# Kernel optimization log

Hardware: AMD Instinct MI355X
Metric: run time of the kernel (lower is better)

The kernel has to match this reference:

```python
import jax, jax.numpy as jnp
import numpy as np

FEAT = 1024
SUPPORT = 512
N = 4096


def setup_inputs() -> dict:
    key = jax.random.key(0)
    k1, k2, k3, k4, k5, k6 = jax.random.split(key, 6)
    s = 1.0 / np.sqrt(FEAT)
    f = jax.random.normal(k1, (N, FEAT), dtype=jnp.float32)
    G = jax.random.normal(k2, (SUPPORT, FEAT), dtype=jnp.float32)
    # PyTorch LSTMCell params: weight_ih [4*hidden, input], weight_hh [4*hidden, hidden]
    W_ih = jax.random.uniform(k3, (4 * FEAT, 2 * FEAT), minval=-s, maxval=s, dtype=jnp.float32)
    W_hh = jax.random.uniform(k4, (4 * FEAT, FEAT), minval=-s, maxval=s, dtype=jnp.float32)
    b_ih = jax.random.uniform(k5, (4 * FEAT,), minval=-s, maxval=s, dtype=jnp.float32)
    b_hh = jax.random.uniform(k6, (4 * FEAT,), minval=-s, maxval=s, dtype=jnp.float32)
    return {"f": f, "G": G, "W_ih": W_ih, "W_hh": W_hh, "b_ih": b_ih, "b_hh": b_hh, "n_ways": 20}


def _lstm_cell(x, h, c, W_ih, W_hh, b_ih, b_hh):
    # gates ordered i, f, g, o as in torch.nn.LSTMCell
    gates = x @ W_ih.T + b_ih + h @ W_hh.T + b_hh  # [N, 4*FEAT]
    i, fg, g, o = jnp.split(gates, 4, axis=1)
    i = jax.nn.sigmoid(i)
    fg = jax.nn.sigmoid(fg)
    g = jnp.tanh(g)
    o = jax.nn.sigmoid(o)
    c_new = fg * c + i * g
    h_new = o * jnp.tanh(c_new)
    return h_new, c_new


def reference(f, G, W_ih, W_hh, b_ih, b_hh, n_ways):
    h = f
    c = jnp.zeros_like(f)  # c_0 expanded, zeros (non-learned Variable)
    for _ in range(n_ways):
        logit_a = h @ G.T                      # [N, M]
        a = jax.nn.softmax(logit_a, axis=0)    # softmax over dim 0, as in original
        r = a @ G                              # [N, FEAT]
        x = jnp.concatenate((f, r), axis=1)    # [N, 2*FEAT]
        h, c = _lstm_cell(x, h, c, W_ih, W_hh, b_ih, b_hh)
        h = h + f
    return h
```

## Files before the change

kernel.cpp:

```cpp
#include <hip/hip_runtime.h>
#include <math.h>

#define NB    4096
#define FEAT  1024
#define MSUP  512
#define G4    4096
#define NWAYS 20

typedef _Float16 f16;
typedef f16 f16x8 __attribute__((ext_vector_type(8)));
typedef f16 f16x4 __attribute__((ext_vector_type(4)));
typedef float f32x4 __attribute__((ext_vector_type(4)));
typedef unsigned int u32;
#define GLOBAL_AS __attribute__((address_space(1)))
#define LDS_AS    __attribute__((address_space(3)))

__device__ __forceinline__ void load_lds16(const void* g, void* l) {
    __builtin_amdgcn_global_load_lds((const GLOBAL_AS u32*)g, (LDS_AS u32*)l, 16, 0, 0);
}

__device__ __forceinline__ float sigm(float x) { return 1.f / (1.f + __expf(-x)); }

template<int BM, int BN, int WROWS, int WCOLS, bool OUTF16, bool HASBIAS>
__global__ __launch_bounds__(256) void mfma_nt(
    void* __restrict__ Cv, int ldc,
    const f16* __restrict__ A1, int lda1, const f16* __restrict__ B1, int ldb1, int K1,
    const f16* __restrict__ A2, int lda2, const f16* __restrict__ B2, int ldb2, int K2,
    const f16* __restrict__ A3, int lda3, const f16* __restrict__ B3, int ldb3, int K3,
    const float* __restrict__ bias)
{
    constexpr int BK = 32;
    constexpr int WM = BM / WROWS, WN = BN / WCOLS;
    constexpr int FM = WM / 16,   FN = WN / 16;
    __shared__ f16 As[BM][BK];
    __shared__ f16 Bs[BN][BK];
    const int tid  = threadIdx.x;
    const int lane = tid & 63;
    const int wrow = (tid >> 6) % WROWS, wcol = (tid >> 6) / WROWS;
    const int bm = blockIdx.y * BM, bn = blockIdx.x * BN;
    const int lr = lane & 15, lq = lane >> 4;

    f32x4 acc[FM][FN] = {};

    #pragma unroll
    for (int pass = 0; pass < 3; ++pass) {
        const f16* A = pass == 0 ? A1 : (pass == 1 ? A2 : A3);
        const f16* B = pass == 0 ? B1 : (pass == 1 ? B2 : B3);
        const int lda = pass == 0 ? lda1 : (pass == 1 ? lda2 : lda3);
        const int ldb = pass == 0 ? ldb1 : (pass == 1 ? ldb2 : ldb3);
        const int K   = pass == 0 ? K1  : (pass == 1 ? K2  : K3);
        if (!A) break;
        #pragma unroll 1
        for (int k0 = 0; k0 < K; k0 += BK) {
            __syncthreads();
            #pragma unroll
            for (int t = 0; t < (BM * 4) / 256; ++t) {
                int c = t * 256 + tid;
                load_lds16(A + (size_t)(bm + (c >> 2)) * lda + k0 + (c & 3) * 8,
                           &As[0][0] + ((size_t)t * 256 + (tid & 192)) * 8);
            }
            #pragma unroll
            for (int t = 0; t < (BN * 4) / 256; ++t) {
                int c = t * 256 + tid;
                load_lds16(B + (size_t)(bn + (c >> 2)) * ldb + k0 + (c & 3) * 8,
                           &Bs[0][0] + ((size_t)t * 256 + (tid & 192)) * 8);
            }
            __syncthreads();
            f16x8 af[FM], bf[FN];
            #pragma unroll
            for (int i = 0; i < FM; ++i)
                af[i] = *(const f16x8*)&As[wrow * WM + i * 16 + lr][lq * 8];
            #pragma unroll
            for (int j = 0; j < FN; ++j)
                bf[j] = *(const f16x8*)&Bs[wcol * WN + j * 16 + lr][lq * 8];
            #pragma unroll
            for (int i = 0; i < FM; ++i)
                #pragma unroll
                for (int j = 0; j < FN; ++j)
                    acc[i][j] = __builtin_amdgcn_mfma_f32_16x16x32_f16(af[i], bf[j], acc[i][j], 0, 0, 0);
        }
    }

    #pragma unroll
    for (int i = 0; i < FM; ++i) {
        #pragma unroll
        for (int j = 0; j < FN; ++j) {
            const int col  = bn + wcol * WN + j * 16 + lr;
            const int row0 = bm + wrow * WM + i * 16 + lq * 4;
            float badd = HASBIAS ? bias[col] : 0.f;
            #pragma unroll
            for (int r = 0; r < 4; ++r) {
                size_t off = (size_t)(row0 + r) * ldc + col;
                float v = acc[i][j][r] + badd;
                if (OUTF16) ((f16*)Cv)[off] = (f16)v;
                else        ((float*)Cv)[off] = v;
            }
        }
    }
}

__global__ __launch_bounds__(512, 2) void gates_8p(
    const f16* __restrict__ a,
    const f16* __restrict__ h,
    const f16* __restrict__ Wcat,
    const f16* __restrict__ pre,
    const float* __restrict__ fin,
    float* __restrict__ cbuf,
    f16* __restrict__ hh,
    float* __restrict__ hout,
    int first, int writeH)
{
    extern __shared__ f16x8 smem8[];
    f16* smem = (f16*)smem8;
    const int tid  = threadIdx.x;
    const int lane = tid & 63;
    const int wid  = tid >> 6;
    const int wrow = wid >> 2, wcol = wid & 3;
    const int lr = lane & 15, lq = lane >> 4;

    const int bidr = blockIdx.y * 16 + blockIdx.x;
    const int wg   = (bidr & 7) * 32 + (bidr >> 3);
    const int bm = (wg >> 4) * 256;
    const int bn = (wg & 15) * 256;

    f32x4 acc[8][4] = {};

    auto stage = [&](const f16* src, int ld, int rb, int ko, f16* lbase, int l) {
        int c = l * 512 + tid;
        int r = c >> 3;
        int x = (c & 7) ^ (r & 7);
        load_lds16(src + (size_t)(rb + r) * ld + ko + (x << 3),
                   lbase + ((size_t)(l * 512 + (tid & 448))) * 8);
    };
    #define RDF(BUF, RB, KK) \
        (*(const f16x8*)((BUF) + ((size_t)((RB) + lr) << 6) + ((((KK) << 2 | lq) ^ (lr & 7)) << 3)))

    #pragma unroll
    for (int l = 0; l < 4; ++l) {
        stage(a,    MSUP, bm, 0, smem,         l);
        stage(Wcat, 2048, bn, 0, smem + 16384, l);
    }

    #pragma unroll 1
    for (int t = 0; t < 32; ++t) {
        f16* Ab = smem + (t & 1) * 32768;
        f16* Bb = Ab + 16384;
        f16* An = smem + ((t + 1) & 1) * 32768;
        f16* Bn = An + 16384;
        const int k1 = (t + 1) * 64;
        const f16* As2 = a; int lda2 = MSUP, ko2 = k1;
        if (k1 >= 1024)     { As2 = h; lda2 = FEAT; ko2 = k1 - 1024; }
        else if (k1 >= 512) { ko2 = k1 - 512; }
        const bool st = (t < 31);

        f16x8 af[4][2], bf[2][2], bg[2][2];

        if (st) {
            stage(As2, lda2, bm, ko2, An, 0);
            stage(Wcat, 2048, bn, k1, Bn, 0);
            asm volatile("s_waitcnt vmcnt(2)" ::: "memory");
        } else {
            asm volatile("s_waitcnt vmcnt(0)" ::: "memory");
        }
        asm volatile("s_barrier" ::: "memory");
        #pragma unroll
        for (int i = 0; i < 4; ++i)
            #pragma unroll
            for (int kk = 0; kk < 2; ++kk)
                af[i][kk] = RDF(Ab, wrow * 128 + i * 16, kk);
        #pragma unroll
        for (int j = 0; j < 2; ++j)
            #pragma unroll
            for (int kk = 0; kk < 2; ++kk)
                bf[j][kk] = RDF(Bb, wcol * 64 + j * 16, kk);
        __builtin_amdgcn_s_setprio(1);
        #pragma unroll
        for (int kk = 0; kk < 2; ++kk)
            #pragma unroll
            for (int i = 0; i < 4; ++i)
                #pragma unroll
                for (int j = 0; j < 2; ++j)
                    acc[i][j] = __builtin_amdgcn_mfma_f32_16x16x32_f16(af[i][kk], bf[j][kk], acc[i][j], 0, 0, 0);
        __builtin_amdgcn_s_setprio(0);
        __builtin_amdgcn_s_barrier();

        if (st) { stage(As2, lda2, bm, ko2, An, 1); stage(Wcat, 2048, bn, k1, Bn, 1); }
        #pragma unroll
        for (int j = 0; j < 2; ++j)
            #pragma unroll
            for (int kk = 0; kk < 2; ++kk)
                bg[j][kk] = RDF(Bb, wcol * 64 + (j + 2) * 16, kk);
        __builtin_amdgcn_s_barrier();
        __builtin_amdgcn_s_setprio(1);
        #pragma unroll
        for (int kk = 0; kk < 2; ++kk)
            #pragma unroll
            for (int i = 0; i < 4; ++i)
                #pragma unroll
                for (int j = 0; j < 2; ++j)
                    acc[i][j + 2] = __builtin_amdgcn_mfma_f32_16x16x32_f16(af[i][kk], bg[j][kk], acc[i][j + 2], 0, 0, 0);
        __builtin_amdgcn_s_setprio(0);
        __builtin_amdgcn_s_barrier();

        if (st) { stage(As2, lda2, bm, ko2, An, 2); stage(Wcat, 2048, bn, k1, Bn, 2); }
        #pragma unroll
        for (int i = 0; i < 4; ++i)
            #pragma unroll
            for (int kk = 0; kk < 2; ++kk)
                af[i][kk] = RDF(Ab, wrow * 128 + (i + 4) * 16, kk);
        __builtin_amdgcn_s_barrier();
        __builtin_amdgcn_s_setprio(1);
        #pragma unroll
        for (int kk = 0; kk < 2; ++kk)
            #pragma unroll
            for (int i = 0; i < 4; ++i)
                #pragma unroll
                for (int j = 0; j < 2; ++j)
                    acc[i + 4][j + 2] = __builtin_amdgcn_mfma_f32_16x16x32_f16(af[i][kk], bg[j][kk], acc[i + 4][j + 2], 0, 0, 0);
        __builtin_amdgcn_s_setprio(0);
        __builtin_amdgcn_s_barrier();

        if (st) { stage(As2, lda2, bm, ko2, An, 3); stage(Wcat, 2048, bn, k1, Bn, 3); }
        #pragma unroll
        for (int j = 0; j < 2; ++j)
            #pragma unroll
            for (int kk = 0; kk < 2; ++kk)
                bf[j][kk] = RDF(Bb, wcol * 64 + j * 16, kk);
        __builtin_amdgcn_s_barrier();
        __builtin_amdgcn_s_setprio(1);
        #pragma unroll
        for (int kk = 0; kk < 2; ++kk)
            #pragma unroll
            for (int i = 0; i < 4; ++i)
                #pragma unroll
                for (int j = 0; j < 2; ++j)
                    acc[i + 4][j] = __builtin_amdgcn_mfma_f32_16x16x32_f16(af[i][kk], bf[j][kk], acc[i + 4][j], 0, 0, 0);
        __builtin_amdgcn_s_setprio(0);
        asm volatile("s_barrier" ::: "memory");
    }
    #undef RDF

    const int q  = lane & 3;
    const int fk = (lane >> 2) & 3;
    #pragma unroll
    for (int i = 0; i < 8; ++i) {
        #pragma unroll
        for (int j = 0; j < 4; ++j) {
            const int cb   = bn + wcol * 64 + j * 16;
            const int row0 = bm + wrow * 128 + i * 16 + lq * 4;
            float x[4];
            #pragma unroll
            for (int r = 0; r < 4; ++r) x[r] = acc[i][j][r];
            float g4[4];
            #pragma unroll
            for (int k = 0; k < 4; ++k) {
                int srcq = (q + k) & 3;
                int src  = (lane & ~3) | srcq;
                g4[srcq] = __shfl(x[(q - k + 4) & 3], src, 64);
            }
            const int row  = row0 + q;
            const int feat = (cb >> 2) + fk;
            f16x4 p = *(const f16x4*)(pre + (size_t)row * G4 + cb + 4 * fk);
            const float i_ = sigm(g4[0] + (float)p[0]);
            const float f_ = sigm(g4[1] + (float)p[1]);
            const float g_ = tanhf(g4[2] + (float)p[2]);
            const float o_ = sigm(g4[3] + (float)p[3]);
            const size_t cid = ((size_t)(blockIdx.y * gridDim.x + blockIdx.x) * 32
                                + i * 4 + j) * 512 + tid;
            float cold = first ? 0.f : cbuf[cid];
            float cn = i_ * g_ + f_ * cold;
            cbuf[cid] = cn;
            float hn = o_ * tanhf(cn) + fin[(size_t)row * FEAT + feat];
            hh[(size_t)row * FEAT + feat] = (f16)hn;
            if (writeH) hout[(size_t)row * FEAT + feat] = hn;
        }
    }
}

__global__ __launch_bounds__(256) void softmax_rows_kernel(
    const float* __restrict__ X, f16* __restrict__ Y)
{
    const int row = blockIdx.x;
    const float* x = X + (size_t)row * NB;
    f16* y = Y + (size_t)row * NB;
    const int tid = threadIdx.x;
    float v[16];
    float mx = -1e30f;
    #pragma unroll
    for (int i = 0; i < 16; ++i) { v[i] = x[tid + (i << 8)]; mx = fmaxf(mx, v[i]); }
    #pragma unroll
    for (int off = 32; off > 0; off >>= 1) mx = fmaxf(mx, __shfl_down(mx, off));
    __shared__ float sm[4];
    if ((tid & 63) == 0) sm[tid >> 6] = mx;
    __syncthreads();
    mx = fmaxf(fmaxf(sm[0], sm[1]), fmaxf(sm[2], sm[3]));
    float s = 0.f;
    #pragma unroll
    for (int i = 0; i < 16; ++i) { v[i] = __expf(v[i] - mx); s += v[i]; }
    #pragma unroll
    for (int off = 32; off > 0; off >>= 1) s += __shfl_down(s, off);
    __shared__ float ss[4];
    if ((tid & 63) == 0) ss[tid >> 6] = s;
    __syncthreads();
    s = ss[0] + ss[1] + ss[2] + ss[3];
    const float inv = 1.f / s;
    #pragma unroll
    for (int i = 0; i < 16; ++i) y[tid + (i << 8)] = (f16)(v[i] * inv);
}

__global__ __launch_bounds__(256) void transpose_f16_kernel(
    const f16* __restrict__ in, f16* __restrict__ out, int R, int C)
{
    __shared__ f16 t[64][65];
    const int r0 = blockIdx.y * 64, c0 = blockIdx.x * 64;
    const int lr = threadIdx.x & 63, lw = threadIdx.x >> 6;
    #pragma unroll
    for (int i = 0; i < 16; ++i) {
        int rr = lw * 16 + i;
        t[rr][lr] = in[(size_t)(r0 + rr) * C + c0 + lr];
    }
    __syncthreads();
    #pragma unroll
    for (int i = 0; i < 16; ++i) {
        int cc = lw * 16 + i;
        out[(size_t)(c0 + cc) * R + r0 + lr] = t[lr][cc];
    }
}

__global__ __launch_bounds__(256) void cvt_f16_kernel(
    const float* __restrict__ in, f16* __restrict__ out, int n)
{
    int idx = (blockIdx.x * 256 + threadIdx.x) * 4;
    if (idx < n) {
        float4 v = *(const float4*)(in + idx);
        f16x4 o = {(f16)v.x, (f16)v.y, (f16)v.z, (f16)v.w};
        *(f16x4*)(out + idx) = o;
    }
}

__global__ __launch_bounds__(256) void cvt_perm_kernel(
    const float* __restrict__ in, f16* __restrict__ out, int ld_in, int ld_out, int col_off)
{
    int idx = (blockIdx.x * 256 + threadIdx.x) * 4;
    int j = idx / ld_in, k = idx % ld_in;
    int dst = 4 * (j & 1023) + (j >> 10);
    float4 v = *(const float4*)(in + idx);
    f16x4 o = {(f16)v.x, (f16)v.y, (f16)v.z, (f16)v.w};
    *(f16x4*)(out + (size_t)dst * ld_out + col_off + k) = o;
}

__global__ __launch_bounds__(256) void bias_perm_kernel(
    const float* __restrict__ bih, const float* __restrict__ bhh, float* __restrict__ out)
{
    int j = blockIdx.x * 256 + threadIdx.x;
    out[4 * (j & 1023) + (j >> 10)] = bih[j] + bhh[j];
}

__global__ __launch_bounds__(256) void split_wcat_kernel(
    const float* __restrict__ in, f16* __restrict__ out)
{
    int idx = (blockIdx.x * 256 + threadIdx.x) * 4;
    int g = idx >> 9, k = idx & 511;
    float4 v = *(const float4*)(in + idx);
    f16x4 hi = {(f16)v.x, (f16)v.y, (f16)v.z, (f16)v.w};
    f16x4 lo = {(f16)(v.x - (float)hi.x), (f16)(v.y - (float)hi.y),
                (f16)(v.z - (float)hi.z), (f16)(v.w - (float)hi.w)};
    *(f16x4*)(out + (size_t)g * 2048 + k) = hi;
    *(f16x4*)(out + (size_t)g * 2048 + 512 + k) = lo;
}

extern "C" void kernel_launch(void* const* d_in, const int* in_sizes, int n_in,
                              void* d_out, int out_size, void* d_ws, size_t ws_size,
                              hipStream_t stream) {
    const float* f   = (const float*)d_in[0];
    const float* G   = (const float*)d_in[1];
    const float* Wih = (const float*)d_in[2];
    const float* Whh = (const float*)d_in[3];
    const float* bih = (const float*)d_in[4];
    const float* bhh = (const float*)d_in[5];
    float* h = (float*)d_out;

    char* W = (char*)d_ws;
    f16*   pre_h   = (f16*)(W);
    float* aT      = (float*)(W + (size_t)(32 << 20));
    f16*   aTh     = (f16*)(W + (size_t)(40 << 20));
    f16*   a_h     = (f16*)(W + (size_t)(44 << 20));
    float* cbuf    = (float*)(W + (size_t)(48 << 20));
    f16*   h0      = (f16*)(W + (size_t)(64 << 20));
    f16*   hA      = (f16*)(W + (size_t)(72 << 20));
    f16*   hB      = (f16*)(W + (size_t)(80 << 20));
    f16*   Wih_h   = (f16*)(W + (size_t)(88 << 20));
    f16*   Wcat    = (f16*)(W + (size_t)(104 << 20));
    float* Wr32    = (float*)(W + (size_t)(120 << 20));
    f16*   G_h     = (f16*)(W + (size_t)(128 << 20));
    float* bias_p  = (float*)(W + (size_t)(129 << 20));

    const f16* NF = nullptr;
    const dim3 blk(256);

    hipFuncSetAttribute((const void*)gates_8p,
                        hipFuncAttributeMaxDynamicSharedMemorySize, 131072);

    cvt_f16_kernel<<<(NB * FEAT) / 1024, blk, 0, stream>>>(f, h0, NB * FEAT);
    cvt_perm_kernel<<<(G4 * 2 * FEAT) / 1024, blk, 0, stream>>>(Wih, Wih_h, 2 * FEAT, 2 * FEAT, 0);
    cvt_perm_kernel<<<(G4 * FEAT) / 1024, blk, 0, stream>>>(Whh, Wcat, FEAT, 2048, 1024);
    cvt_f16_kernel<<<(MSUP * FEAT) / 1024, blk, 0, stream>>>(G, G_h, MSUP * FEAT);
    bias_perm_kernel<<<G4 / 256, blk, 0, stream>>>(bih, bhh, bias_p);

    mfma_nt<128, 128, 2, 2, true, true><<<dim3(G4 / 128, NB / 128), blk, 0, stream>>>(
        pre_h, G4,
        h0, FEAT, Wih_h, 2 * FEAT, FEAT,
        NF, 0, NF, 0, 0, NF, 0, NF, 0, 0,
        bias_p);

    mfma_nt<128, 128, 2, 2, false, false><<<dim3(MSUP / 128, G4 / 128), blk, 0, stream>>>(
        Wr32, MSUP,
        Wih_h + FEAT, 2 * FEAT, G_h, FEAT, FEAT,
        NF, 0, NF, 0, 0, NF, 0, NF, 0, 0,
        nullptr);
    split_wcat_kernel<<<(G4 * MSUP) / 1024, blk, 0, stream>>>(Wr32, Wcat);

    const f16* hcur = h0;
    for (int it = 0; it < NWAYS; ++it) {
        mfma_nt<64, 64, 2, 2, false, false><<<dim3(NB / 64, MSUP / 64), blk, 0, stream>>>(
            aT, NB,
            G_h, FEAT, hcur, FEAT, FEAT,
            NF, 0, NF, 0, 0, NF, 0, NF, 0, 0,
            nullptr);

        softmax_rows_kernel<<<MSUP, blk, 0, stream>>>(aT, aTh);
        transpose_f16_kernel<<<dim3(NB / 64, MSUP / 64), blk, 0, stream>>>(aTh, a_h, MSUP, NB);

        f16* hnext = (it & 1) ? hB : hA;
        gates_8p<<<dim3(G4 / 256, NB / 256), 512, 131072, stream>>>(
            a_h, hcur, Wcat, pre_h, f, cbuf, hnext, h, it == 0, it == NWAYS - 1);
        hcur = hnext;
    }
}
```

Before: 2.435 ms.

## Reschedule gate GEMM prefetch stages and waitcnts across MFMA phases

Reorders the global-to-LDS prefetch of the next K tile in the fused LSTM gate GEMM. B (weight) chunks are issued early and A chunks later, and the vmcnt waits move to mid-iteration and end of iteration instead of the start. Sched barriers pin the ordering. The aim is to hide global load latency behind more MFMA work and cut stalls at the top of each iteration, at the cost of more carefully tuned waitcnt counts that could race if they are miscounted.

After: 2.436 ms. Within noise of the previous version (+0.0%).

```diff
diff --git a/kernel.cpp b/kernel.cpp
--- a/kernel.cpp
+++ b/kernel.cpp
@@ -134,12 +134,16 @@
     };
     #define RDF(BUF, RB, KK) \
         (*(const f16x8*)((BUF) + ((size_t)((RB) + lr) << 6) + ((((KK) << 2 | lq) ^ (lr & 7)) << 3)))
+    #define BAR()  asm volatile("s_barrier" ::: "memory")
+    #define SBAR() __builtin_amdgcn_sched_barrier(0)
 
     #pragma unroll
     for (int l = 0; l < 4; ++l) {
+        stage(Wcat, 2048, bn, 0, smem + 16384, l);
         stage(a,    MSUP, bm, 0, smem,         l);
-        stage(Wcat, 2048, bn, 0, smem + 16384, l);
-    }
+    }
+    asm volatile("s_waitcnt vmcnt(0)" ::: "memory");
+    BAR();
 
     #pragma unroll 1
     for (int t = 0; t < 32; ++t) {
@@ -155,14 +159,6 @@
 
         f16x8 af[4][2], bf[2][2], bg[2][2];
 
-        if (st) {
-            stage(As2, lda2, bm, ko2, An, 0);
-            stage(Wcat, 2048, bn, k1, Bn, 0);
-            asm volatile("s_waitcnt vmcnt(2)" ::: "memory");
-        } else {
-            asm volatile("s_waitcnt vmcnt(0)" ::: "memory");
-        }
-        asm volatile("s_barrier" ::: "memory");
         #pragma unroll
         for (int i = 0; i < 4; ++i)
             #pragma unroll
@@ -173,6 +169,12 @@
             #pragma unroll
             for (int kk = 0; kk < 2; ++kk)
                 bf[j][kk] = RDF(Bb, wcol * 64 + j * 16, kk);
+        if (st) {
+            stage(Wcat, 2048, bn, k1, Bn, 0);
+            stage(Wcat, 2048, bn, k1, Bn, 1);
+            stage(Wcat, 2048, bn, k1, Bn, 2);
+        }
+        BAR(); SBAR();
         __builtin_amdgcn_s_setprio(1);
         #pragma unroll
         for (int kk = 0; kk < 2; ++kk)
@@ -182,15 +184,19 @@
                 for (int j = 0; j < 2; ++j)
                     acc[i][j] = __builtin_amdgcn_mfma_f32_16x16x32_f16(af[i][kk], bf[j][kk], acc[i][j], 0, 0, 0);
         __builtin_amdgcn_s_setprio(0);
-        __builtin_amdgcn_s_barrier();
-
-        if (st) { stage(As2, lda2, bm, ko2, An, 1); stage(Wcat, 2048, bn, k1, Bn, 1); }
+        BAR();
+
         #pragma unroll
         for (int j = 0; j < 2; ++j)
             #pragma unroll
             for (int kk = 0; kk < 2; ++kk)
                 bg[j][kk] = RDF(Bb, wcol * 64 + (j + 2) * 16, kk);
-        __builtin_amdgcn_s_barrier();
+        if (st) {
+            stage(Wcat, 2048, bn, k1, Bn, 3);
+            stage(As2, lda2, bm, ko2, An, 0);
+            stage(As2, lda2, bm, ko2, An, 2);
+        }
+        BAR(); SBAR();
         __builtin_amdgcn_s_setprio(1);
         #pragma unroll
         for (int kk = 0; kk < 2; ++kk)
@@ -200,15 +206,20 @@
                 for (int j = 0; j < 2; ++j)
                     acc[i][j + 2] = __builtin_amdgcn_mfma_f32_16x16x32_f16(af[i][kk], bg[j][kk], acc[i][j + 2], 0, 0, 0);
         __builtin_amdgcn_s_setprio(0);
-        __builtin_amdgcn_s_barrier();
-
-        if (st) { stage(As2, lda2, bm, ko2, An, 2); stage(Wcat, 2048, bn, k1, Bn, 2); }
+        if (st) asm volatile("s_waitcnt vmcnt(6)" ::: "memory");
+        else    asm volatile("s_waitcnt vmcnt(0)" ::: "memory");
+        BAR();
+
         #pragma unroll
         for (int i = 0; i < 4; ++i)
             #pragma unroll
             for (int kk = 0; kk < 2; ++kk)
                 af[i][kk] = RDF(Ab, wrow * 128 + (i + 4) * 16, kk);
-        __builtin_amdgcn_s_barrier();
+        if (st) {
+            stage(As2, lda2, bm, ko2, An, 1);
+            stage(As2, lda2, bm, ko2, An, 3);
+        }
+        BAR(); SBAR();
         __builtin_amdgcn_s_setprio(1);
         #pragma unroll
         for (int kk = 0; kk < 2; ++kk)
@@ -218,15 +229,14 @@
                 for (int j = 0; j < 2; ++j)
                     acc[i + 4][j + 2] = __builtin_amdgcn_mfma_f32_16x16x32_f16(af[i][kk], bg[j][kk], acc[i + 4][j + 2], 0, 0, 0);
         __builtin_amdgcn_s_setprio(0);
-        __builtin_amdgcn_s_barrier();
-
-        if (st) { stage(As2, lda2, bm, ko2, An, 3); stage(Wcat, 2048, bn, k1, Bn, 3); }
+        BAR();
+
         #pragma unroll
         for (int j = 0; j < 2; ++j)
             #pragma unroll
             for (int kk = 0; kk < 2; ++kk)
                 bf[j][kk] = RDF(Bb, wcol * 64 + j * 16, kk);
-        __builtin_amdgcn_s_barrier();
+        BAR(); SBAR();
         __builtin_amdgcn_s_setprio(1);
         #pragma unroll
         for (int kk = 0; kk < 2; ++kk)
@@ -236,7 +246,8 @@
                 for (int j = 0; j < 2; ++j)
                     acc[i + 4][j] = __builtin_amdgcn_mfma_f32_16x16x32_f16(af[i][kk], bf[j][kk], acc[i + 4][j], 0, 0, 0);
         __builtin_amdgcn_s_setprio(0);
-        asm volatile("s_barrier" ::: "memory");
+        if (st) asm volatile("s_waitcnt vmcnt(2)" ::: "memory");
+        BAR();
     }
     #undef RDF
 
```

## Replace 256x256 8-phase gates GEMM with simpler 128x128 double-buffered kernel

Applied to the files above, without the earlier changes.

Shrinks the fused gates GEMM tile from 256x256 with 8 waves to 128x128 with 4 waves. It also replaces the hand-interleaved 8-phase schedule (setprio, split barriers, partial vmcnt waits) with a plain double-buffer loop: load fragments, issue the next tile's LDS loads, run the MFMAs, then sync. The grid grows to 1024 blocks and LDS per block is halved, raising occupancy. The cost is lower data reuse per tile, more global traffic, and less fine-grained overlap of loads with MFMAs.

After: 2.632 ms. 8.1% more time.

```diff
diff --git a/kernel.cpp b/kernel.cpp
--- a/kernel.cpp
+++ b/kernel.cpp
@@ -99,7 +99,8 @@
     }
 }
 
-__global__ __launch_bounds__(512, 2) void gates_8p(
+template<int DUMMY>
+__global__ __launch_bounds__(256, 2) void gates_mp(
     const f16* __restrict__ a,
     const f16* __restrict__ h,
     const f16* __restrict__ Wcat,
@@ -115,139 +116,84 @@
     const int tid  = threadIdx.x;
     const int lane = tid & 63;
     const int wid  = tid >> 6;
-    const int wrow = wid >> 2, wcol = wid & 3;
+    const int wrow = wid >> 1, wcol = wid & 1;
     const int lr = lane & 15, lq = lane >> 4;
 
-    const int bidr = blockIdx.y * 16 + blockIdx.x;
-    const int wg   = (bidr & 7) * 32 + (bidr >> 3);
-    const int bm = (wg >> 4) * 256;
-    const int bn = (wg & 15) * 256;
-
-    f32x4 acc[8][4] = {};
+    const int bidr = blockIdx.y * 32 + blockIdx.x;
+    const int wg   = (bidr & 7) * 128 + (bidr >> 3);
+    const int bm = (wg >> 5) * 128;
+    const int bn = (wg & 31) * 128;
+
+    f32x4 acc[4][4] = {};
 
     auto stage = [&](const f16* src, int ld, int rb, int ko, f16* lbase, int l) {
-        int c = l * 512 + tid;
+        int c = l * 256 + tid;
         int r = c >> 3;
         int x = (c & 7) ^ (r & 7);
         load_lds16(src + (size_t)(rb + r) * ld + ko + (x << 3),
-                   lbase + ((size_t)(l * 512 + (tid & 448))) * 8);
+                   lbase + ((size_t)(l * 256 + (tid & 192))) * 8);
     };
     #define RDF(BUF, RB, KK) \
         (*(const f16x8*)((BUF) + ((size_t)((RB) + lr) << 6) + ((((KK) << 2 | lq) ^ (lr & 7)) << 3)))
 
     #pragma unroll
     for (int l = 0; l < 4; ++l) {
-        stage(a,    MSUP, bm, 0, smem,         l);
-        stage(Wcat, 2048, bn, 0, smem + 16384, l);
-    }
+        stage(a,    MSUP, bm, 0, smem,        l);
+        stage(Wcat, 2048, bn, 0, smem + 8192, l);
+    }
+    __syncthreads();
 
     #pragma unroll 1
     for (int t = 0; t < 32; ++t) {
-        f16* Ab = smem + (t & 1) * 32768;
-        f16* Bb = Ab + 16384;
-        f16* An = smem + ((t + 1) & 1) * 32768;
-        f16* Bn = An + 16384;
+        f16* Ab = smem + (t & 1) * 16384;
+        f16* Bb = Ab + 8192;
+        f16* An = smem + ((t + 1) & 1) * 16384;
+        f16* Bn = An + 8192;
         const int k1 = (t + 1) * 64;
         const f16* As2 = a; int lda2 = MSUP, ko2 = k1;
         if (k1 >= 1024)     { As2 = h; lda2 = FEAT; ko2 = k1 - 1024; }
         else if (k1 >= 512) { ko2 = k1 - 512; }
-        const bool st = (t < 31);
-
-        f16x8 af[4][2], bf[2][2], bg[2][2];
-
-        if (st) {
-            stage(As2, lda2, bm, ko2, An, 0);
-            stage(Wcat, 2048, bn, k1, Bn, 0);
-            asm volatile("s_waitcnt vmcnt(2)" ::: "memory");
-        } else {
-            asm volatile("s_waitcnt vmcnt(0)" ::: "memory");
-        }
-        asm volatile("s_barrier" ::: "memory");
+
+        f16x8 af[4][2], bf[4][2];
         #pragma unroll
         for (int i = 0; i < 4; ++i)
             #pragma unroll
             for (int kk = 0; kk < 2; ++kk)
-                af[i][kk] = RDF(Ab, wrow * 128 + i * 16, kk);
-        #pragma unroll
-        for (int j = 0; j < 2; ++j)
+                af[i][kk] = RDF(Ab, wrow * 64 + i * 16, kk);
+        #pragma unroll
+        for (int j = 0; j < 4; ++j)
             #pragma unroll
             for (int kk = 0; kk < 2; ++kk)
                 bf[j][kk] = RDF(Bb, wcol * 64 + j * 16, kk);
-        __builtin_amdgcn_s_setprio(1);
+
+        if (t < 31) {
+            #pragma unroll
+            for (int l = 0; l < 4; ++l) {
+                stage(As2, lda2, bm, ko2, An, l);
+                stage(Wcat, 2048, bn, k1, Bn, l);
+            }
+        }
+
         #pragma unroll
         for (int kk = 0; kk < 2; ++kk)
             #pragma unroll
             for (int i = 0; i < 4; ++i)
                 #pragma unroll
-                for (int j = 0; j < 2; ++j)
+                for (int j = 0; j < 4; ++j)
                     acc[i][j] = __builtin_amdgcn_mfma_f32_16x16x32_f16(af[i][kk], bf[j][kk], acc[i][j], 0, 0, 0);
-        __builtin_amdgcn_s_setprio(0);
-        __builtin_amdgcn_s_barrier();
-
-        if (st) { stage(As2, lda2, bm, ko2, An, 1); stage(Wcat, 2048, bn, k1, Bn, 1); }
-        #pragma unroll
-        for (int j = 0; j < 2; ++j)
-            #pragma unroll
-            for (int kk = 0; kk < 2; ++kk)
-                bg[j][kk] = RDF(Bb, wcol * 64 + (j + 2) * 16, kk);
-        __builtin_amdgcn_s_barrier();
-        __builtin_amdgcn_s_setprio(1);
-        #pragma unroll
-        for (int kk = 0; kk < 2; ++kk)
-            #pragma unroll
-            for (int i = 0; i < 4; ++i)
-                #pragma unroll
-                for (int j = 0; j < 2; ++j)
-                    acc[i][j + 2] = __builtin_amdgcn_mfma_f32_16x16x32_f16(af[i][kk], bg[j][kk], acc[i][j + 2], 0, 0, 0);
-        __builtin_amdgcn_s_setprio(0);
-        __builtin_amdgcn_s_barrier();
-
-        if (st) { stage(As2, lda2, bm, ko2, An, 2); stage(Wcat, 2048, bn, k1, Bn, 2); }
-        #pragma unroll
-        for (int i = 0; i < 4; ++i)
-            #pragma unroll
-            for (int kk = 0; kk < 2; ++kk)
-                af[i][kk] = RDF(Ab, wrow * 128 + (i + 4) * 16, kk);
-        __builtin_amdgcn_s_barrier();
-        __builtin_amdgcn_s_setprio(1);
-        #pragma unroll
-        for (int kk = 0; kk < 2; ++kk)
-            #pragma unroll
-            for (int i = 0; i < 4; ++i)
-                #pragma unroll
-                for (int j = 0; j < 2; ++j)
-                    acc[i + 4][j + 2] = __builtin_amdgcn_mfma_f32_16x16x32_f16(af[i][kk], bg[j][kk], acc[i + 4][j + 2], 0, 0, 0);
-        __builtin_amdgcn_s_setprio(0);
-        __builtin_amdgcn_s_barrier();
-
-        if (st) { stage(As2, lda2, bm, ko2, An, 3); stage(Wcat, 2048, bn, k1, Bn, 3); }
-        #pragma unroll
-        for (int j = 0; j < 2; ++j)
-            #pragma unroll
-            for (int kk = 0; kk < 2; ++kk)
-                bf[j][kk] = RDF(Bb, wcol * 64 + j * 16, kk);
-        __builtin_amdgcn_s_barrier();
-        __builtin_amdgcn_s_setprio(1);
-        #pragma unroll
-        for (int kk = 0; kk < 2; ++kk)
-            #pragma unroll
-            for (int i = 0; i < 4; ++i)
-                #pragma unroll
-                for (int j = 0; j < 2; ++j)
-                    acc[i + 4][j] = __builtin_amdgcn_mfma_f32_16x16x32_f16(af[i][kk], bf[j][kk], acc[i + 4][j], 0, 0, 0);
-        __builtin_amdgcn_s_setprio(0);
-        asm volatile("s_barrier" ::: "memory");
+
+        __syncthreads();
     }
     #undef RDF
 
     const int q  = lane & 3;
     const int fk = (lane >> 2) & 3;
     #pragma unroll
-    for (int i = 0; i < 8; ++i) {
+    for (int i = 0; i < 4; ++i) {
         #pragma unroll
         for (int j = 0; j < 4; ++j) {
             const int cb   = bn + wcol * 64 + j * 16;
-            const int row0 = bm + wrow * 128 + i * 16 + lq * 4;
+            const int row0 = bm + wrow * 64 + i * 16 + lq * 4;
             float x[4];
             #pragma unroll
             for (int r = 0; r < 4; ++r) x[r] = acc[i][j][r];
@@ -265,8 +211,8 @@
             const float f_ = sigm(g4[1] + (float)p[1]);
             const float g_ = tanhf(g4[2] + (float)p[2]);
             const float o_ = sigm(g4[3] + (float)p[3]);
-            const size_t cid = ((size_t)(blockIdx.y * gridDim.x + blockIdx.x) * 32
-                                + i * 4 + j) * 512 + tid;
+            const size_t cid = ((size_t)(blockIdx.y * gridDim.x + blockIdx.x) * 16
+                                + i * 4 + j) * 256 + tid;
             float cold = first ? 0.f : cbuf[cid];
             float cn = i_ * g_ + f_ * cold;
             cbuf[cid] = cn;
@@ -398,8 +344,8 @@
     const f16* NF = nullptr;
     const dim3 blk(256);
 
-    hipFuncSetAttribute((const void*)gates_8p,
-                        hipFuncAttributeMaxDynamicSharedMemorySize, 131072);
+    hipFuncSetAttribute((const void*)gates_mp<0>,
+                        hipFuncAttributeMaxDynamicSharedMemorySize, 65536);
 
     cvt_f16_kernel<<<(NB * FEAT) / 1024, blk, 0, stream>>>(f, h0, NB * FEAT);
     cvt_perm_kernel<<<(G4 * 2 * FEAT) / 1024, blk, 0, stream>>>(Wih, Wih_h, 2 * FEAT, 2 * FEAT, 0);
@@ -432,7 +378,7 @@
         transpose_f16_kernel<<<dim3(NB / 64, MSUP / 64), blk, 0, stream>>>(aTh, a_h, MSUP, NB);
 
         f16* hnext = (it & 1) ? hB : hA;
-        gates_8p<<<dim3(G4 / 256, NB / 256), 512, 131072, stream>>>(
+        gates_mp<0><<<dim3(32, 32), 256, 65536, stream>>>(
             a_h, hcur, Wcat, pre_h, f, cbuf, hnext, h, it == 0, it == NWAYS - 1);
         hcur = hnext;
     }
```
